# Performance work log

Measured on AMD Instinct MI355X. Metric: run time of the kernel, lower is better.

The kernel has to match this reference:

```python
import jax, jax.numpy as jnp
import numpy as np

C_IN, C_OUT, K, PAD, STRIDE = 128, 256, 3, 1, 1
H = W = 256


def setup_inputs() -> dict:
    key = jax.random.key(0)
    k1, k2, k3 = jax.random.split(key, 3)
    # batch=1: the original forward uses X_pad[0] for every batch index,
    # so with m=1 the buggy loop and a standard conv are mathematically identical.
    x = jax.random.normal(k1, (1, C_IN, H, W), dtype=jnp.float32)
    # nn.Parameter(torch.rand(...)) -> uniform[0,1)
    weight = jax.random.uniform(k2, (C_OUT, C_IN, K, K), dtype=jnp.float32)
    bias = jax.random.uniform(k3, (C_OUT,), dtype=jnp.float32)
    return {"x": x, "weight": weight, "bias": bias}


def reference(x, weight, bias):
    # Faithful math of convAppx.forward with FP_appx_mul treated as exact
    # multiply (FP_appx_mul is not defined in the source): a plain 2D
    # cross-correlation (no kernel flip, matching the sliced elementwise
    # product) with symmetric padding, stride 1, plus per-channel bias.
    z = jax.lax.conv_general_dilated(
        x, weight,
        window_strides=(STRIDE, STRIDE),
        padding=((PAD, PAD), (PAD, PAD)),
        dimension_numbers=("NCHW", "OIHW", "NCHW"),
    )
    return z + bias[None, :, None, None]
```

## Files before the change

kernel.cpp:

```cpp
#include <hip/hip_runtime.h>
#include <hip/hip_bf16.h>


typedef short bf16x8 __attribute__((ext_vector_type(8)));
typedef float f32x4 __attribute__((ext_vector_type(4)));
typedef int   i32x4 __attribute__((ext_vector_type(4)));
typedef unsigned short u16x4 __attribute__((ext_vector_type(4)));
typedef unsigned short u16x8 __attribute__((ext_vector_type(8)));

#define CIN   128
#define COUT  256
#define HH    256
#define WW    256
#define HP    258
#define ROWP  (HP * CIN)

static __device__ __forceinline__ unsigned short f2bf(float v) {
    __hip_bfloat16 b = __float2bfloat16(v);
    return *reinterpret_cast<unsigned short*>(&b);
}

static __device__ __forceinline__ void gload_lds16(const unsigned short* g, unsigned short* l) {
    __builtin_amdgcn_global_load_lds(
        (const __attribute__((address_space(1))) unsigned int*)g,
        (__attribute__((address_space(3))) unsigned int*)l, 16, 0, 0);
}

template<int CTRL>
static __device__ __forceinline__ bf16x8 rotf(bf16x8 a) {
    i32x4 ai = __builtin_bit_cast(i32x4, a);
    i32x4 r;
    #pragma unroll
    for (int j = 0; j < 4; ++j)
        r[j] = __builtin_amdgcn_mov_dpp(ai[j], CTRL, 0xF, 0xF, true);
    return __builtin_bit_cast(bf16x8, r);
}
#define ROR_P1 0x12F
#define ROR_P2 0x12E

__global__ __launch_bounds__(256) void prep_kernel(const float* __restrict__ x,
                                                   const float* __restrict__ w,
                                                   unsigned short* __restrict__ xb,
                                                   unsigned short* __restrict__ wr) {
    int bid = blockIdx.x;
    int t   = threadIdx.x;

    if (bid < 65) {
        int i = bid * 256 + t;
        if (i < 16448) {
            u16x8 z = {0, 0, 0, 0, 0, 0, 0, 0};
            int off;
            if (i < 8256) {
                int r   = (i >= 4128) ? 1 : 0;
                int rem = i - r * 4128;
                off = (r * 257) * ROWP + rem * 8;
            } else {
                int j   = i - 8256;
                int col = j >> 12;
                int rem = j & 4095;
                int hp  = (rem >> 4) + 1;
                int c8  = rem & 15;
                off = hp * ROWP + (col * 257) * CIN + c8 * 8;
            }
            *(u16x8*)(&xb[off]) = z;
        }
    }

    if (bid < 128) {
        int p = bid * 256 + t;
        const float* src = w + p * 9;
        #pragma unroll
        for (int khw = 0; khw < 9; ++khw)
            wr[khw * (COUT * CIN) + p] = f2bf(src[khw]);
    }

    int h  = bid >> 2;
    int w0 = (bid & 3) * 64;
    __shared__ unsigned short tile[CIN * 72];

    int wq  = t & 15;
    int cib = t >> 4;
    for (int c0 = 0; c0 < CIN; c0 += 16) {
        int ci = c0 + cib;
        float4 v = *(const float4*)(x + ci * (HH * WW) + h * WW + w0 + wq * 4);
        u16x4 p;
        p.x = f2bf(v.x); p.y = f2bf(v.y); p.z = f2bf(v.z); p.w = f2bf(v.w);
        *(u16x4*)(&tile[ci * 72 + wq * 4]) = p;
    }
    __syncthreads();

    for (int it = 0; it < 4; ++it) {
        int idx = it * 256 + t;
        int ww_ = idx & 63;
        int c8  = idx >> 6;
        u16x8 o;
        #pragma unroll
        for (int j = 0; j < 8; ++j)
            o[j] = tile[(c8 * 8 + j) * 72 + ww_];
        int dst = ((h + 1) * HP + (w0 + ww_ + 1)) * CIN + c8 * 8;
        *(u16x8*)(&xb[dst]) = o;
    }
}

__global__ __launch_bounds__(256, 2) void conv_mfma_kernel(const unsigned short* __restrict__ xb,
                                                           const unsigned short* __restrict__ wr,
                                                           const float* __restrict__ bias,
                                                           float* __restrict__ out) {
    __shared__ unsigned short A0[128 * 64];
    __shared__ unsigned short A1[128 * 64];
    __shared__ unsigned short A2[128 * 64];
    __shared__ unsigned short Bs[256 * 64];

    int bid   = blockIdx.x;
    int inner = bid >> 3;
    int h     = (bid & 7) * 32 + (inner >> 1);
    int co0   = (inner & 1) * 128;

    int t    = threadIdx.x;
    int lane = t & 63;
    int wave = t >> 6;
    int wm   = wave >> 1;
    int wn   = wave & 1;
    int quad = lane >> 4;
    int l16  = lane & 15;

    f32x4 acc[4][8];
    #pragma unroll
    for (int mi = 0; mi < 4; ++mi)
        #pragma unroll
        for (int ni = 0; ni < 8; ++ni)
            acc[mi][ni] = (f32x4){0.f, 0.f, 0.f, 0.f};

    unsigned short* const Ap[3] = {A0, A1, A2};

    #pragma unroll 1
    for (int i = 0; i < 6; ++i) {
        int kh     = i >> 1;
        int cihalf = i & 1;

        #pragma unroll
        for (int p = 0; p < 3; ++p) {
            const unsigned short* wsrc =
                wr + (size_t)(kh * 3 + p) * (COUT * CIN) + co0 * CIN + cihalf * 64;
            unsigned short* dst = Ap[p];
            #pragma unroll
            for (int it = 0; it < 4; ++it) {
                int seg = it * 256 + t;
                int r   = seg >> 3;
                int s   = seg & 7;
                int c   = s ^ (r & 7);
                gload_lds16(wsrc + r * CIN + c * 8, &dst[seg * 8]);
            }
        }
        {
            const unsigned short* xrow = xb + (size_t)(h + kh) * ROWP + cihalf * 64;
            #pragma unroll
            for (int it = 0; it < 8; ++it) {
                int seg = it * 256 + t;
                int sc  = seg >> 3;
                int s   = seg & 7;
                int c   = s ^ (sc & 7);
                gload_lds16(xrow + (sc + 1) * CIN + c * 8, &Bs[seg * 8]);
            }
        }
        asm volatile("s_waitcnt vmcnt(0)" ::: "memory");
        __builtin_amdgcn_s_barrier();
        __builtin_amdgcn_sched_barrier(0);

        #pragma unroll
        for (int kk = 0; kk < 2; ++kk) {
            int ck  = kk * 4 + quad;
            int asl = (ck ^ (l16 & 7)) * 8;

            bf16x8 af0[4], af1[4], af2[4];
            #pragma unroll
            for (int mi = 0; mi < 4; ++mi) {
                int ro = (wm * 64 + mi * 16 + l16) * 64;
                af0[mi] = *(const bf16x8*)(&A0[ro + asl]);
                af1[mi] = *(const bf16x8*)(&A1[ro + asl]);
                af2[mi] = *(const bf16x8*)(&A2[ro + asl]);
            }

            auto rdB = [&](int ni_) -> bf16x8 {
                int pc  = wn * 128 + ni_ * 16 + l16;
                int sc  = pc - 1;
                int scc = sc < 0 ? 0 : (sc > 255 ? 255 : sc);
                bf16x8 v = *(const bf16x8*)(&Bs[scc * 64 + ((ck ^ (scc & 7)) * 8)]);
                if (pc < 1 || pc > 256) {
                    bf16x8 z = {0, 0, 0, 0, 0, 0, 0, 0};
                    v = z;
                }
                return v;
            };

            bf16x8 cur = rdB(0);
            #pragma unroll
            for (int ni = 0; ni < 8; ++ni) {
                bf16x8 nxt = rdB(ni + 1);
                bf16x8 r1c = rotf<ROR_P1>(cur), r1n = rotf<ROR_P1>(nxt);
                bf16x8 s1  = (l16 == 15) ? r1n : r1c;
                bf16x8 r2c = rotf<ROR_P2>(cur), r2n = rotf<ROR_P2>(nxt);
                bf16x8 s2  = (l16 >= 14) ? r2n : r2c;

                __builtin_amdgcn_s_setprio(1);
                #pragma unroll
                for (int mi = 0; mi < 4; ++mi)
                    acc[mi][ni] = __builtin_amdgcn_mfma_f32_16x16x32_bf16(
                        af0[mi], cur, acc[mi][ni], 0, 0, 0);
                #pragma unroll
                for (int mi = 0; mi < 4; ++mi)
                    acc[mi][ni] = __builtin_amdgcn_mfma_f32_16x16x32_bf16(
                        af1[mi], s1, acc[mi][ni], 0, 0, 0);
                #pragma unroll
                for (int mi = 0; mi < 4; ++mi)
                    acc[mi][ni] = __builtin_amdgcn_mfma_f32_16x16x32_bf16(
                        af2[mi], s2, acc[mi][ni], 0, 0, 0);
                __builtin_amdgcn_s_setprio(0);
                cur = nxt;
            }
        }
        __builtin_amdgcn_s_barrier();
        __builtin_amdgcn_sched_barrier(0);
    }

    int sp0 = wn * 128 + l16;
    #pragma unroll
    for (int mi = 0; mi < 4; ++mi) {
        #pragma unroll
        for (int r = 0; r < 4; ++r) {
            int co = co0 + wm * 64 + mi * 16 + quad * 4 + r;
            float b = bias[co];
            float* orow = out + (size_t)co * (HH * WW) + h * WW + sp0;
            #pragma unroll
            for (int ni = 0; ni < 8; ++ni)
                orow[ni * 16] = acc[mi][ni][r] + b;
        }
    }
}

extern "C" void kernel_launch(void* const* d_in, const int* in_sizes, int n_in,
                              void* d_out, int out_size, void* d_ws, size_t ws_size,
                              hipStream_t stream) {
    const float* x    = (const float*)d_in[0];
    const float* w    = (const float*)d_in[1];
    const float* bias = (const float*)d_in[2];
    float* out        = (float*)d_out;

    unsigned short* xb = (unsigned short*)d_ws;
    unsigned short* wr = xb + (size_t)HP * HP * CIN;

    prep_kernel<<<dim3(1024), dim3(256), 0, stream>>>(x, w, xb, wr);
    conv_mfma_kernel<<<dim3(512), dim3(256), 0, stream>>>(xb, wr, bias, out);
}
```

Measured before the change: 144.6 us.

## Halve conv block tile and K-chunk to raise occupancy and grid size

Each block now covers 128 output columns instead of 256, and the channel loop moves in 32-channel chunks over 12 steps instead of 64-channel chunks over 6. Per-wave accumulators shrink from 4x8 to 2x8 tiles, and the LDS swizzle and the padding-column handling in the B tile are reworked. The grid doubles to 1024 blocks and launch bounds ask for 4 blocks per CU, aiming for more latency hiding. In exchange the kernel has more barriers, more weight reloads, and less MFMA work per LDS load.

```diff
diff --git a/kernel.cpp b/kernel.cpp
--- a/kernel.cpp
+++ b/kernel.cpp
@@ -102,95 +102,93 @@
     }
 }
 
-__global__ __launch_bounds__(256, 2) void conv_mfma_kernel(const unsigned short* __restrict__ xb,
+__global__ __launch_bounds__(256, 4) void conv_mfma_kernel(const unsigned short* __restrict__ xb,
                                                            const unsigned short* __restrict__ wr,
                                                            const float* __restrict__ bias,
                                                            float* __restrict__ out) {
-    __shared__ unsigned short A0[128 * 64];
-    __shared__ unsigned short A1[128 * 64];
-    __shared__ unsigned short A2[128 * 64];
-    __shared__ unsigned short Bs[256 * 64];
+    __shared__ unsigned short A0[128 * 32];
+    __shared__ unsigned short A1[128 * 32];
+    __shared__ unsigned short A2[128 * 32];
+    __shared__ unsigned short Bs[130 * 32];
 
     int bid   = blockIdx.x;
     int inner = bid >> 3;
-    int h     = (bid & 7) * 32 + (inner >> 1);
+    int h     = (bid & 7) * 32 + (inner >> 2);
     int co0   = (inner & 1) * 128;
+    int s0    = ((inner >> 1) & 1) * 128;
 
     int t    = threadIdx.x;
     int lane = t & 63;
     int wave = t >> 6;
-    int wm   = wave >> 1;
-    int wn   = wave & 1;
     int quad = lane >> 4;
     int l16  = lane & 15;
 
-    f32x4 acc[4][8];
+    f32x4 acc[2][8];
     #pragma unroll
-    for (int mi = 0; mi < 4; ++mi)
+    for (int mi = 0; mi < 2; ++mi)
         #pragma unroll
         for (int ni = 0; ni < 8; ++ni)
             acc[mi][ni] = (f32x4){0.f, 0.f, 0.f, 0.f};
 
-    unsigned short* const Ap[3] = {A0, A1, A2};
-
     #pragma unroll 1
-    for (int i = 0; i < 6; ++i) {
-        int kh     = i >> 1;
-        int cihalf = i & 1;
-
-        #pragma unroll
-        for (int p = 0; p < 3; ++p) {
-            const unsigned short* wsrc =
-                wr + (size_t)(kh * 3 + p) * (COUT * CIN) + co0 * CIN + cihalf * 64;
-            unsigned short* dst = Ap[p];
-            #pragma unroll
-            for (int it = 0; it < 4; ++it) {
+    for (int i = 0; i < 12; ++i) {
+        int kh  = i >> 2;
+        int ciq = i & 3;
+
+        {
+            const unsigned short* wbase =
+                wr + (size_t)(kh * 3) * (COUT * CIN) + co0 * CIN + ciq * 32;
+            #pragma unroll
+            for (int it = 0; it < 2; ++it) {
                 int seg = it * 256 + t;
-                int r   = seg >> 3;
-                int s   = seg & 7;
-                int c   = s ^ (r & 7);
-                gload_lds16(wsrc + r * CIN + c * 8, &dst[seg * 8]);
+                int r   = seg >> 2;
+                int s   = seg & 3;
+                int c   = s ^ ((r >> 1) & 3);
+                const unsigned short* src = wbase + r * CIN + c * 8;
+                gload_lds16(src,                    &A0[seg * 8]);
+                gload_lds16(src + (COUT * CIN),     &A1[seg * 8]);
+                gload_lds16(src + 2 * (COUT * CIN), &A2[seg * 8]);
             }
         }
         {
-            const unsigned short* xrow = xb + (size_t)(h + kh) * ROWP + cihalf * 64;
-            #pragma unroll
-            for (int it = 0; it < 8; ++it) {
+            const unsigned short* xrow = xb + (size_t)(h + kh) * ROWP + ciq * 32;
+            #pragma unroll
+            for (int it = 0; it < 2; ++it) {
                 int seg = it * 256 + t;
-                int sc  = seg >> 3;
-                int s   = seg & 7;
-                int c   = s ^ (sc & 7);
-                gload_lds16(xrow + (sc + 1) * CIN + c * 8, &Bs[seg * 8]);
+                int lc  = seg >> 2;
+                int s   = seg & 3;
+                int c   = s ^ ((lc >> 1) & 3);
+                gload_lds16(xrow + (s0 + lc) * CIN + c * 8, &Bs[seg * 8]);
+            }
+            if (t < 8) {
+                int seg = 512 + t;
+                int lc  = seg >> 2;
+                int s   = seg & 3;
+                int c   = s ^ ((lc >> 1) & 3);
+                gload_lds16(xrow + (s0 + lc) * CIN + c * 8, &Bs[seg * 8]);
             }
         }
         asm volatile("s_waitcnt vmcnt(0)" ::: "memory");
         __builtin_amdgcn_s_barrier();
         __builtin_amdgcn_sched_barrier(0);
 
-        #pragma unroll
-        for (int kk = 0; kk < 2; ++kk) {
-            int ck  = kk * 4 + quad;
-            int asl = (ck ^ (l16 & 7)) * 8;
-
-            bf16x8 af0[4], af1[4], af2[4];
-            #pragma unroll
-            for (int mi = 0; mi < 4; ++mi) {
-                int ro = (wm * 64 + mi * 16 + l16) * 64;
-                af0[mi] = *(const bf16x8*)(&A0[ro + asl]);
-                af1[mi] = *(const bf16x8*)(&A1[ro + asl]);
-                af2[mi] = *(const bf16x8*)(&A2[ro + asl]);
+        {
+            int ck = quad;
+
+            bf16x8 af0[2], af1[2], af2[2];
+            #pragma unroll
+            for (int mi = 0; mi < 2; ++mi) {
+                int row = wave * 32 + mi * 16 + l16;
+                int ro  = row * 32 + (ck ^ ((row >> 1) & 3)) * 8;
+                af0[mi] = *(const bf16x8*)(&A0[ro]);
+                af1[mi] = *(const bf16x8*)(&A1[ro]);
+                af2[mi] = *(const bf16x8*)(&A2[ro]);
             }
 
             auto rdB = [&](int ni_) -> bf16x8 {
-                int pc  = wn * 128 + ni_ * 16 + l16;
-                int sc  = pc - 1;
-                int scc = sc < 0 ? 0 : (sc > 255 ? 255 : sc);
-                bf16x8 v = *(const bf16x8*)(&Bs[scc * 64 + ((ck ^ (scc & 7)) * 8)]);
-                if (pc < 1 || pc > 256) {
-                    bf16x8 z = {0, 0, 0, 0, 0, 0, 0, 0};
-                    v = z;
-                }
-                return v;
+                int lc = ni_ * 16 + l16;
+                if (lc > 129) lc = 129;
+                return *(const bf16x8*)(&Bs[lc * 32 + ((ck ^ ((lc >> 1) & 3)) * 8)]);
             };
 
             bf16x8 cur = rdB(0);
@@ -204,15 +202,15 @@
 
                 __builtin_amdgcn_s_setprio(1);
                 #pragma unroll
-                for (int mi = 0; mi < 4; ++mi)
+                for (int mi = 0; mi < 2; ++mi)
                     acc[mi][ni] = __builtin_amdgcn_mfma_f32_16x16x32_bf16(
                         af0[mi], cur, acc[mi][ni], 0, 0, 0);
                 #pragma unroll
-                for (int mi = 0; mi < 4; ++mi)
+                for (int mi = 0; mi < 2; ++mi)
                     acc[mi][ni] = __builtin_amdgcn_mfma_f32_16x16x32_bf16(
                         af1[mi], s1, acc[mi][ni], 0, 0, 0);
                 #pragma unroll
-                for (int mi = 0; mi < 4; ++mi)
+                for (int mi = 0; mi < 2; ++mi)
                     acc[mi][ni] = __builtin_amdgcn_mfma_f32_16x16x32_bf16(
                         af2[mi], s2, acc[mi][ni], 0, 0, 0);
                 __builtin_amdgcn_s_setprio(0);
@@ -223,14 +221,13 @@
         __builtin_amdgcn_sched_barrier(0);
     }
 
-    int sp0 = wn * 128 + l16;
     #pragma unroll
-    for (int mi = 0; mi < 4; ++mi) {
+    for (int mi = 0; mi < 2; ++mi) {
         #pragma unroll
         for (int r = 0; r < 4; ++r) {
-            int co = co0 + wm * 64 + mi * 16 + quad * 4 + r;
+            int co = co0 + wave * 32 + mi * 16 + quad * 4 + r;
             float b = bias[co];
-            float* orow = out + (size_t)co * (HH * WW) + h * WW + sp0;
+            float* orow = out + (size_t)co * (HH * WW) + h * WW + s0 + l16;
             #pragma unroll
             for (int ni = 0; ni < 8; ++ni)
                 orow[ni * 16] = acc[mi][ni][r] + b;
@@ -250,5 +247,5 @@
     unsigned short* wr = xb + (size_t)HP * HP * CIN;
 
     prep_kernel<<<dim3(1024), dim3(256), 0, stream>>>(x, w, xb, wr);
-    conv_mfma_kernel<<<dim3(512), dim3(256), 0, stream>>>(xb, wr, bias, out);
-}
+    conv_mfma_kernel<<<dim3(1024), dim3(256), 0, stream>>>(xb, wr, bias, out);
+}
```

Result: faster. 139.5 us (-3.5%).
